# Performance work log

Hardware: AMD Instinct MI355X
Metric: run time of the kernel (lower is better)

Reference implementation:

```python
import jax, jax.numpy as jnp
import numpy as np

N = 50000       # nodes
E = 800000      # edges (avg degree 16)
C_IN = 128
C_HID = 64
C_OUT = 64
NEG_SLOPE = 0.2  # PyG GATConv default


def setup_inputs() -> dict:
    key = jax.random.key(0)
    ks = jax.random.split(key, 20)
    inp = {
        "x": jax.random.normal(ks[0], (N, C_IN), dtype=jnp.float32),
        "edge_index": jax.random.randint(ks[1], (2, E), 0, N, dtype=jnp.int32),
        "batch_size": N,
        "framework": 1,
    }
    dims = [(C_IN, C_HID), (C_HID, C_HID), (C_HID, C_OUT)]
    k = 2
    for i, (cin, cout) in enumerate(dims):
        s = 1.0 / np.sqrt(cin)
        inp[f"W{i}"] = jax.random.normal(ks[k], (cin, cout), jnp.float32) * s; k += 1
        inp[f"a_src{i}"] = jax.random.normal(ks[k], (cout,), jnp.float32) * (1.0 / np.sqrt(cout)); k += 1
        inp[f"a_dst{i}"] = jax.random.normal(ks[k], (cout,), jnp.float32) * (1.0 / np.sqrt(cout)); k += 1
        inp[f"b{i}"] = jnp.zeros((cout,), jnp.float32); k += 1
    return inp


def _gat_conv(h, src, dst, n, W, a_src, a_dst, b):
    # h: [n, cin] -> [n, cout]; single head, PyG GATConv semantics
    hp = h @ W                                   # [n, cout]
    alpha_s = hp @ a_src                         # [n]
    alpha_d = hp @ a_dst                         # [n]
    e = alpha_s[src] + alpha_d[dst]              # [E'] per-edge logits
    e = jnp.where(e > 0, e, NEG_SLOPE * e)       # leaky_relu(0.2)
    # segment softmax over incoming edges of each destination node
    m = jax.ops.segment_max(e, dst, num_segments=n)
    e = jnp.exp(e - m[dst])
    denom = jax.ops.segment_sum(e, dst, num_segments=n)
    a = e / (denom[dst] + 1e-16)                 # [E']
    msg = hp[src] * a[:, None]                   # [E', cout]
    out = jax.ops.segment_sum(msg, dst, num_segments=n)
    return out + b


def reference(x, edge_index, batch_size, framework,
              W0, a_src0, a_dst0, b0,
              W1, a_src1, a_dst1, b1,
              W2, a_src2, a_dst2, b2):
    n = x.shape[0]
    loops = jnp.arange(n, dtype=edge_index.dtype)  # PyG add_self_loops=True
    src = jnp.concatenate([edge_index[0], loops])
    dst = jnp.concatenate([edge_index[1], loops])
    params = [(W0, a_src0, a_dst0, b0), (W1, a_src1, a_dst1, b1), (W2, a_src2, a_dst2, b2)]
    h = x
    for W, a_s, a_d, b in params:
        h = jax.nn.relu(_gat_conv(h, src, dst, n, W, a_s, a_d, b))
    if framework:
        return h
    return h[:batch_size]
```

## Files before the change

### kernel.cpp

```cpp
#include <hip/hip_runtime.h>
#include <hip/hip_fp16.h>
#include <math.h>

#define NEG_SLOPE 0.2f
#define BSHIFT 8
#define BCAP 8192

typedef __attribute__((ext_vector_type(8))) short bf16x8;
typedef __attribute__((ext_vector_type(4))) float f32x4;

__device__ __forceinline__ float leaky(float e) {
    return e > 0.f ? e : NEG_SLOPE * e;
}
__device__ __forceinline__ float to_f(float x) { return x; }
__device__ __forceinline__ float to_f(__half x) { return __half2float(x); }


__global__ __launch_bounds__(256) void partition_kernel(
        const int* __restrict__ src, const int* __restrict__ dst,
        int* __restrict__ bucketLen, int* __restrict__ pairs, int E, int nbk) {
    __shared__ int cnt[256];
    __shared__ int run[256];
    int t = threadIdx.x;
    int chunk = (E + gridDim.x - 1) / gridDim.x;
    int beg = blockIdx.x * chunk;
    int end = min(beg + chunk, E);
    cnt[t] = 0;
    __syncthreads();
    for (int i = beg + t; i < end; i += 256)
        atomicAdd(&cnt[dst[i] >> BSHIFT], 1);
    __syncthreads();
    if (t < nbk) run[t] = t * BCAP + atomicAdd(&bucketLen[t], cnt[t]);
    __syncthreads();
    for (int i = beg + t; i < end; i += 256) {
        int d = dst[i];
        int slot = atomicAdd(&run[d >> BSHIFT], 1);
        if (slot < (d >> BSHIFT) * BCAP + BCAP)
            pairs[slot] = (src[i] << BSHIFT) | (d & 255);
    }
}

__global__ __launch_bounds__(256) void csr_build_kernel(
        const int* __restrict__ bucketLen, const int* __restrict__ pairs,
        int* __restrict__ off, int* __restrict__ degA,
        int* __restrict__ csr_src, int N, int nbk) {
    __shared__ int degl[256];
    __shared__ int s[256];
    __shared__ int cur[256];
    int t = threadIdx.x;
    int b = blockIdx.x;
    int n0 = b << BSHIFT;
    int nodecnt = min(256, N - n0);
    int ebeg = b * BCAP;
    int eend = ebeg + bucketLen[b];

    degl[t] = 0;
    __syncthreads();
    for (int i = ebeg + t; i < eend; i += 256)
        atomicAdd(&degl[pairs[i] & 255], 1);
    __syncthreads();

    int v = degl[t];
    s[t] = v;
    __syncthreads();
    for (int o = 1; o < 256; o <<= 1) {
        int x = (t >= o) ? s[t - o] : 0;
        __syncthreads();
        s[t] += x;
        __syncthreads();
    }
    int excl = s[t] - v;
    if (t < nodecnt) {
        off[n0 + t] = ebeg + excl;
        degA[n0 + t] = v;
    }
    cur[t] = excl;
    __syncthreads();

    for (int i = ebeg + t; i < eend; i += 256) {
        int pk = pairs[i];
        int p = atomicAdd(&cur[pk & 255], 1);
        csr_src[ebeg + p] = pk >> BSHIFT;
    }
}


__device__ __forceinline__ unsigned f2bf_bits(float x) {
    unsigned u = __float_as_uint(x);
    return (u + 0x7fffu + ((u >> 16) & 1u)) >> 16;
}

__global__ __launch_bounds__(256) void pack_w3_kernel(
        const float* __restrict__ W0, const float* __restrict__ W1,
        const float* __restrict__ W2, short* __restrict__ Whi,
        short* __restrict__ Wlo, int* __restrict__ bucketLen) {
    int idx = blockIdx.x * 256 + threadIdx.x;
    if (idx < 256) bucketLen[idx] = 0;
    if (idx >= 16384) return;
    const float* W;
    int base, li;
    if (idx < 8192)       { W = W0; base = 0;     li = idx; }
    else if (idx < 12288) { W = W1; base = 8192;  li = idx - 8192; }
    else                  { W = W2; base = 12288; li = idx - 12288; }
    int k = li >> 6, col = li & 63;
    int c = k >> 5, kin = k & 31;
    int g = col >> 4, nn = col & 15;
    float x = W[li];
    unsigned hb = f2bf_bits(x);
    float hf = __uint_as_float(hb << 16);
    unsigned lb = f2bf_bits(x - hf);
    int o = base + (((c * 4 + g) * 16 + nn) << 5) + kin;
    Whi[o] = (short)hb;
    Wlo[o] = (short)lb;
}


template <int CIN, typename InT>
__global__ __launch_bounds__(256) void gemm_mfma_kernel(
        const InT* __restrict__ h, const short* __restrict__ Whi,
        const short* __restrict__ Wlo,
        const float* __restrict__ a_src, const float* __restrict__ a_dst,
        __half* __restrict__ hp, float* __restrict__ as_, float* __restrict__ ad_,
        int n) {
    constexpr int KC = CIN / 32;
    int t = threadIdx.x, wave = t >> 6, lane = t & 63;
    int quad = lane >> 4, l16 = lane & 15;
    int node0 = blockIdx.x * 64 + wave * 16;

    f32x4 acc[4];
#pragma unroll
    for (int g = 0; g < 4; ++g) acc[g] = (f32x4){0.f, 0.f, 0.f, 0.f};

    int nodeA = node0 + l16;
    bool va = nodeA < n;
    const InT* hrow = h + (size_t)(va ? nodeA : 0) * CIN + quad * 8;

#pragma unroll
    for (int c = 0; c < KC; ++c) {
        bf16x8 bhi[4], blo[4];
#pragma unroll
        for (int g = 0; g < 4; ++g) {
            int o = (((c * 4 + g) * 16 + l16) << 5) + quad * 8;
            bhi[g] = *(const bf16x8*)(Whi + o);
            blo[g] = *(const bf16x8*)(Wlo + o);
        }
        bf16x8 ahi, alo;
#pragma unroll
        for (int j = 0; j < 8; ++j) {
            float x = va ? to_f(hrow[c * 32 + j]) : 0.f;
            unsigned hb = f2bf_bits(x);
            float hf = __uint_as_float(hb << 16);
            unsigned lb = f2bf_bits(x - hf);
            ahi[j] = (short)hb;
            alo[j] = (short)lb;
        }
#pragma unroll
        for (int g = 0; g < 4; ++g) {
            acc[g] = __builtin_amdgcn_mfma_f32_16x16x32_bf16(ahi, bhi[g], acc[g], 0, 0, 0);
            acc[g] = __builtin_amdgcn_mfma_f32_16x16x32_bf16(ahi, blo[g], acc[g], 0, 0, 0);
            acc[g] = __builtin_amdgcn_mfma_f32_16x16x32_bf16(alo, bhi[g], acc[g], 0, 0, 0);
        }
    }

    float as4[4], ad4[4];
#pragma unroll
    for (int g = 0; g < 4; ++g) {
        as4[g] = a_src[g * 16 + l16];
        ad4[g] = a_dst[g * 16 + l16];
    }
#pragma unroll
    for (int r = 0; r < 4; ++r) {
        int node = node0 + quad * 4 + r;
        bool v = node < n;
        float vs = 0.f, vd = 0.f;
#pragma unroll
        for (int g = 0; g < 4; ++g) {
            float val = acc[g][r];
            if (v) hp[(size_t)node * 64 + g * 16 + l16] = __float2half_rn(val);
            vs = fmaf(val, as4[g], vs);
            vd = fmaf(val, ad4[g], vd);
        }
#pragma unroll
        for (int o = 1; o <= 8; o <<= 1) {
            vs += __shfl_xor(vs, o);
            vd += __shfl_xor(vd, o);
        }
        if (v && l16 == 0) {
            as_[node] = vs;
            ad_[node] = vd;
        }
    }
}


__device__ __forceinline__ void h4_to_f(uint2 u, float* f) {
    __half2 a = *(__half2*)&u.x;
    __half2 b = *(__half2*)&u.y;
    float2 f01 = __half22float2(a);
    float2 f23 = __half22float2(b);
    f[0] = f01.x; f[1] = f01.y; f[2] = f23.x; f[3] = f23.y;
}

__device__ __forceinline__ void store_row(float* out, size_t idx, float4 r) {
    ((float4*)out)[idx] = r;
}
__device__ __forceinline__ void store_row(__half* out, size_t idx, float4 r) {
    __half2 a = __floats2half2_rn(r.x, r.y);
    __half2 b = __floats2half2_rn(r.z, r.w);
    uint2 u;
    u.x = *(unsigned*)&a;
    u.y = *(unsigned*)&b;
    ((uint2*)out)[idx] = u;
}
__device__ __forceinline__ void store_el(float* out, size_t idx, float v) { out[idx] = v; }
__device__ __forceinline__ void store_el(__half* out, size_t idx, float v) { out[idx] = __float2half_rn(v); }

template <typename OutT>
__global__ __launch_bounds__(256) void agg_kernel(
        const __half* __restrict__ hp,
        const float* __restrict__ as_, const float* __restrict__ ad_,
        const int* __restrict__ off, const int* __restrict__ degA,
        const int* __restrict__ csr_src,
        const float* __restrict__ bias, OutT* __restrict__ out, int n) {
    __shared__ float pw[4][64];
    __shared__ int ps[4][64];
    int t = threadIdx.x;
    int wave = t >> 6, lane = t & 63;
    int node = blockIdx.x * 4 + wave;
    if (node >= n) return;

    int beg = off[node];
    int deg = degA[node];
    int end = beg + deg;
    float adst = ad_[node];
    float e_self = leaky(as_[node] + adst);

    if (deg <= 64) {
        bool valid = lane < deg;
        int s = valid ? csr_src[beg + lane] : 0;
        float e = valid ? leaky(as_[s] + adst) : -3.4e38f;

        float m = e;
#pragma unroll
        for (int o = 32; o > 0; o >>= 1) m = fmaxf(m, __shfl_xor(m, o));
        m = fmaxf(m, e_self);

        float p = valid ? __expf(e - m) : 0.f;
        float pself = __expf(e_self - m);
        float se = p;
#pragma unroll
        for (int o = 32; o > 0; o >>= 1) se += __shfl_xor(se, o);
        se += pself;
        float inv = 1.0f / (se + 1e-16f);
        p *= inv;

        pw[wave][lane] = p;
        ps[wave][lane] = s;

        int group = lane >> 4, sub = lane & 15;
        const uint2* hp2 = (const uint2*)hp;

        float wself = (group == 0) ? pself * inv : 0.f;
        float hv[4];
        h4_to_f(hp2[(size_t)node * 16 + sub], hv);
        float ax = wself * hv[0], ay = wself * hv[1];
        float az = wself * hv[2], aw = wself * hv[3];

        int j = group;
        float w0 = 0.f, w1 = 0.f;
        uint2 u0 = make_uint2(0u, 0u), u1 = make_uint2(0u, 0u);
        if (j < deg) {
            w0 = pw[wave][j];
            u0 = hp2[(size_t)ps[wave][j] * 16 + sub];
        }
        if (j + 4 < deg) {
            w1 = pw[wave][j + 4];
            u1 = hp2[(size_t)ps[wave][j + 4] * 16 + sub];
        }
        for (; j + 8 < deg; j += 4) {
            float w2 = pw[wave][j + 8];
            uint2 u2 = hp2[(size_t)ps[wave][j + 8] * 16 + sub];
            float f[4];
            h4_to_f(u0, f);
            ax = fmaf(w0, f[0], ax);
            ay = fmaf(w0, f[1], ay);
            az = fmaf(w0, f[2], az);
            aw = fmaf(w0, f[3], aw);
            w0 = w1; u0 = u1;
            w1 = w2; u1 = u2;
        }
        if (j < deg) {
            float f[4];
            h4_to_f(u0, f);
            ax = fmaf(w0, f[0], ax);
            ay = fmaf(w0, f[1], ay);
            az = fmaf(w0, f[2], az);
            aw = fmaf(w0, f[3], aw);
        }
        if (j + 4 < deg) {
            float f[4];
            h4_to_f(u1, f);
            ax = fmaf(w1, f[0], ax);
            ay = fmaf(w1, f[1], ay);
            az = fmaf(w1, f[2], az);
            aw = fmaf(w1, f[3], aw);
        }

#pragma unroll
        for (int o = 16; o <= 32; o <<= 1) {
            ax += __shfl_xor(ax, o);
            ay += __shfl_xor(ay, o);
            az += __shfl_xor(az, o);
            aw += __shfl_xor(aw, o);
        }

        float4 b4 = ((const float4*)bias)[sub];
        float4 r;
        r.x = ax + b4.x; r.x = r.x > 0.f ? r.x : 0.f;
        r.y = ay + b4.y; r.y = r.y > 0.f ? r.y : 0.f;
        r.z = az + b4.z; r.z = r.z > 0.f ? r.z : 0.f;
        r.w = aw + b4.w; r.w = r.w > 0.f ? r.w : 0.f;
        if (group == 0) store_row(out, (size_t)node * 16 + sub, r);
    } else {
        float mymax = e_self;
        for (int i = beg + lane; i < end; i += 64) {
            int s = csr_src[i];
            mymax = fmaxf(mymax, leaky(as_[s] + adst));
        }
#pragma unroll
        for (int o = 32; o > 0; o >>= 1) mymax = fmaxf(mymax, __shfl_xor(mymax, o));
        float m = mymax;

        float se = 0.f;
        for (int i = beg + lane; i < end; i += 64) {
            int s = csr_src[i];
            se += __expf(leaky(as_[s] + adst) - m);
        }
#pragma unroll
        for (int o = 32; o > 0; o >>= 1) se += __shfl_xor(se, o);
        se += __expf(e_self - m);
        float inv = 1.0f / (se + 1e-16f);

        float acc = __expf(e_self - m) * inv * __half2float(hp[(size_t)node * 64 + lane]);
        for (int i = beg; i < end; ++i) {
            int s = csr_src[i];
            float w = __expf(leaky(as_[s] + adst) - m) * inv;
            acc = fmaf(w, __half2float(hp[(size_t)s * 64 + lane]), acc);
        }
        float r = acc + bias[lane];
        store_el(out, (size_t)node * 64 + lane, r > 0.f ? r : 0.f);
    }
}


extern "C" void kernel_launch(void* const* d_in, const int* in_sizes, int n_in,
                              void* d_out, int out_size, void* d_ws, size_t ws_size,
                              hipStream_t stream) {
    const float* x = (const float*)d_in[0];
    const int* edge_index = (const int*)d_in[1];
    const int N = in_sizes[0] / 128;
    const int E = in_sizes[1] / 2;
    const int NBK = (N + 255) >> BSHIFT;

    const float* W[3]    = {(const float*)d_in[4], (const float*)d_in[8],  (const float*)d_in[12]};
    const float* asrc[3] = {(const float*)d_in[5], (const float*)d_in[9],  (const float*)d_in[13]};
    const float* adst[3] = {(const float*)d_in[6], (const float*)d_in[10], (const float*)d_in[14]};
    const float* bias[3] = {(const float*)d_in[7], (const float*)d_in[11], (const float*)d_in[15]};

    char* ws = (char*)d_ws;
    size_t o = 0;
    auto alloc = [&](size_t bytes) {
        char* p = ws + o;
        o += (bytes + 255) & ~(size_t)255;
        return p;
    };
    int* bucketLen    = (int*)alloc(256 * 4);
    int* pairs        = (int*)alloc((size_t)NBK * BCAP * 4);
    int* off          = (int*)alloc((size_t)N * 4);
    int* degA         = (int*)alloc((size_t)N * 4);
    int* csr_src      = (int*)alloc((size_t)NBK * BCAP * 4);
    float* as_        = (float*)alloc((size_t)N * 4);
    float* ad_        = (float*)alloc((size_t)N * 4);
    __half* hpbuf     = (__half*)alloc((size_t)N * 64 * 2);
    __half* actB      = (__half*)alloc((size_t)N * 64 * 2);
    short* Whi        = (short*)alloc(16384 * 2);
    short* Wlo        = (short*)alloc(16384 * 2);

    const int* srcp = edge_index;
    const int* dstp = edge_index + E;

    pack_w3_kernel<<<64, 256, 0, stream>>>(W[0], W[1], W[2], Whi, Wlo, bucketLen);
    partition_kernel<<<256, 256, 0, stream>>>(srcp, dstp, bucketLen, pairs, E, NBK);
    csr_build_kernel<<<NBK, 256, 0, stream>>>(bucketLen, pairs, off, degA, csr_src, N, NBK);

    int gb = (N + 63) / 64;
    int ab = (N + 3) / 4;

    gemm_mfma_kernel<128, float><<<gb, 256, 0, stream>>>(
        x, Whi, Wlo, asrc[0], adst[0], hpbuf, as_, ad_, N);
    agg_kernel<__half><<<ab, 256, 0, stream>>>(
        hpbuf, as_, ad_, off, degA, csr_src, bias[0], actB, N);

    gemm_mfma_kernel<64, __half><<<gb, 256, 0, stream>>>(
        actB, Whi + 8192, Wlo + 8192, asrc[1], adst[1], hpbuf, as_, ad_, N);
    agg_kernel<__half><<<ab, 256, 0, stream>>>(
        hpbuf, as_, ad_, off, degA, csr_src, bias[1], actB, N);

    gemm_mfma_kernel<64, __half><<<gb, 256, 0, stream>>>(
        actB, Whi + 12288, Wlo + 12288, asrc[2], adst[2], hpbuf, as_, ad_, N);
    agg_kernel<float><<<ab, 256, 0, stream>>>(
        hpbuf, as_, ad_, off, degA, csr_src, bias[2], (float*)d_out, N);
}
```

Before: 272.7 us.

## Fuse CSR build with first GEMM, use half-wave per node in aggregation

Merges the CSR build and the first-layer GEMM into one launch, with blocks split by index so the two independent jobs run side by side. The aggregation kernel now gives each node 32 lanes instead of 64, handling 8 nodes per block, and issues four gathers per step for more memory-level parallelism. The high-degree fallback loads half2 pairs, and the partition grid grows from 256 to 1024 blocks. Half-wave nodes use fewer lanes per gather, and nodes with more than 32 in-edges drop to the slower serial path.

```diff
diff --git a/kernel.cpp b/kernel.cpp
--- a/kernel.cpp
+++ b/kernel.cpp
@@ -40,15 +40,14 @@
     }
 }
 
-__global__ __launch_bounds__(256) void csr_build_kernel(
-        const int* __restrict__ bucketLen, const int* __restrict__ pairs,
+__device__ void csr_build_body(
+        int b, const int* __restrict__ bucketLen, const int* __restrict__ pairs,
         int* __restrict__ off, int* __restrict__ degA,
-        int* __restrict__ csr_src, int N, int nbk) {
+        int* __restrict__ csr_src, int N) {
     __shared__ int degl[256];
     __shared__ int s[256];
     __shared__ int cur[256];
     int t = threadIdx.x;
-    int b = blockIdx.x;
     int n0 = b << BSHIFT;
     int nodecnt = min(256, N - n0);
     int ebeg = b * BCAP;
@@ -116,8 +115,8 @@
 
 
 template <int CIN, typename InT>
-__global__ __launch_bounds__(256) void gemm_mfma_kernel(
-        const InT* __restrict__ h, const short* __restrict__ Whi,
+__device__ void gemm_body(
+        int bid, const InT* __restrict__ h, const short* __restrict__ Whi,
         const short* __restrict__ Wlo,
         const float* __restrict__ a_src, const float* __restrict__ a_dst,
         __half* __restrict__ hp, float* __restrict__ as_, float* __restrict__ ad_,
@@ -125,7 +124,7 @@
     constexpr int KC = CIN / 32;
     int t = threadIdx.x, wave = t >> 6, lane = t & 63;
     int quad = lane >> 4, l16 = lane & 15;
-    int node0 = blockIdx.x * 64 + wave * 16;
+    int node0 = bid * 64 + wave * 16;
 
     f32x4 acc[4];
 #pragma unroll
@@ -190,6 +189,31 @@
             ad_[node] = vd;
         }
     }
+}
+
+__global__ __launch_bounds__(256) void csr_gemm0_kernel(
+        const int* __restrict__ bucketLen, const int* __restrict__ pairs,
+        int* __restrict__ off, int* __restrict__ degA, int* __restrict__ csr_src,
+        int N, int nbk,
+        const float* __restrict__ x, const short* __restrict__ Whi,
+        const short* __restrict__ Wlo, const float* __restrict__ a_src,
+        const float* __restrict__ a_dst, __half* __restrict__ hp,
+        float* __restrict__ as_, float* __restrict__ ad_) {
+    if ((int)blockIdx.x < nbk)
+        csr_build_body(blockIdx.x, bucketLen, pairs, off, degA, csr_src, N);
+    else
+        gemm_body<128, float>((int)blockIdx.x - nbk, x, Whi, Wlo, a_src, a_dst,
+                              hp, as_, ad_, N);
+}
+
+template <int CIN, typename InT>
+__global__ __launch_bounds__(256) void gemm_mfma_kernel(
+        const InT* __restrict__ h, const short* __restrict__ Whi,
+        const short* __restrict__ Wlo,
+        const float* __restrict__ a_src, const float* __restrict__ a_dst,
+        __half* __restrict__ hp, float* __restrict__ as_, float* __restrict__ ad_,
+        int n) {
+    gemm_body<CIN, InT>((int)blockIdx.x, h, Whi, Wlo, a_src, a_dst, hp, as_, ad_, n);
 }
 
 
@@ -226,7 +250,8 @@
     __shared__ int ps[4][64];
     int t = threadIdx.x;
     int wave = t >> 6, lane = t & 63;
-    int node = blockIdx.x * 4 + wave;
+    int hf = lane >> 5, l32 = lane & 31;
+    int node = blockIdx.x * 8 + wave * 2 + hf;
     if (node >= n) return;
 
     int beg = off[node];
@@ -235,21 +260,21 @@
     float adst = ad_[node];
     float e_self = leaky(as_[node] + adst);
 
-    if (deg <= 64) {
-        bool valid = lane < deg;
-        int s = valid ? csr_src[beg + lane] : 0;
+    if (deg <= 32) {
+        bool valid = l32 < deg;
+        int s = valid ? csr_src[beg + l32] : 0;
         float e = valid ? leaky(as_[s] + adst) : -3.4e38f;
 
         float m = e;
 #pragma unroll
-        for (int o = 32; o > 0; o >>= 1) m = fmaxf(m, __shfl_xor(m, o));
+        for (int o = 16; o > 0; o >>= 1) m = fmaxf(m, __shfl_xor(m, o));
         m = fmaxf(m, e_self);
 
         float p = valid ? __expf(e - m) : 0.f;
         float pself = __expf(e_self - m);
         float se = p;
 #pragma unroll
-        for (int o = 32; o > 0; o >>= 1) se += __shfl_xor(se, o);
+        for (int o = 16; o > 0; o >>= 1) se += __shfl_xor(se, o);
         se += pself;
         float inv = 1.0f / (se + 1e-16f);
         p *= inv;
@@ -257,7 +282,7 @@
         pw[wave][lane] = p;
         ps[wave][lane] = s;
 
-        int group = lane >> 4, sub = lane & 15;
+        int group = l32 >> 4, sub = l32 & 15;
         const uint2* hp2 = (const uint2*)hp;
 
         float wself = (group == 0) ? pself * inv : 0.f;
@@ -266,53 +291,33 @@
         float ax = wself * hv[0], ay = wself * hv[1];
         float az = wself * hv[2], aw = wself * hv[3];
 
-        int j = group;
-        float w0 = 0.f, w1 = 0.f;
-        uint2 u0 = make_uint2(0u, 0u), u1 = make_uint2(0u, 0u);
-        if (j < deg) {
-            w0 = pw[wave][j];
-            u0 = hp2[(size_t)ps[wave][j] * 16 + sub];
-        }
-        if (j + 4 < deg) {
-            w1 = pw[wave][j + 4];
-            u1 = hp2[(size_t)ps[wave][j + 4] * 16 + sub];
-        }
-        for (; j + 8 < deg; j += 4) {
-            float w2 = pw[wave][j + 8];
-            uint2 u2 = hp2[(size_t)ps[wave][j + 8] * 16 + sub];
-            float f[4];
-            h4_to_f(u0, f);
-            ax = fmaf(w0, f[0], ax);
-            ay = fmaf(w0, f[1], ay);
-            az = fmaf(w0, f[2], az);
-            aw = fmaf(w0, f[3], aw);
-            w0 = w1; u0 = u1;
-            w1 = w2; u1 = u2;
-        }
-        if (j < deg) {
-            float f[4];
-            h4_to_f(u0, f);
-            ax = fmaf(w0, f[0], ax);
-            ay = fmaf(w0, f[1], ay);
-            az = fmaf(w0, f[2], az);
-            aw = fmaf(w0, f[3], aw);
-        }
-        if (j + 4 < deg) {
-            float f[4];
-            h4_to_f(u1, f);
-            ax = fmaf(w1, f[0], ax);
-            ay = fmaf(w1, f[1], ay);
-            az = fmaf(w1, f[2], az);
-            aw = fmaf(w1, f[3], aw);
-        }
-
-#pragma unroll
-        for (int o = 16; o <= 32; o <<= 1) {
-            ax += __shfl_xor(ax, o);
-            ay += __shfl_xor(ay, o);
-            az += __shfl_xor(az, o);
-            aw += __shfl_xor(aw, o);
-        }
+        int base = hf * 32;
+        for (int j = group; j < deg; j += 8) {
+            float w4[4];
+            uint2 u4[4];
+#pragma unroll
+            for (int q = 0; q < 4; ++q) {
+                int jj = j + 2 * q;
+                bool ok = jj < deg;
+                w4[q] = ok ? pw[wave][base + jj] : 0.f;
+                u4[q] = ok ? hp2[(size_t)ps[wave][base + jj] * 16 + sub]
+                           : make_uint2(0u, 0u);
+            }
+#pragma unroll
+            for (int q = 0; q < 4; ++q) {
+                float f[4];
+                h4_to_f(u4[q], f);
+                ax = fmaf(w4[q], f[0], ax);
+                ay = fmaf(w4[q], f[1], ay);
+                az = fmaf(w4[q], f[2], az);
+                aw = fmaf(w4[q], f[3], aw);
+            }
+        }
+
+        ax += __shfl_xor(ax, 16);
+        ay += __shfl_xor(ay, 16);
+        az += __shfl_xor(az, 16);
+        aw += __shfl_xor(aw, 16);
 
         float4 b4 = ((const float4*)bias)[sub];
         float4 r;
@@ -323,32 +328,39 @@
         if (group == 0) store_row(out, (size_t)node * 16 + sub, r);
     } else {
         float mymax = e_self;
-        for (int i = beg + lane; i < end; i += 64) {
+        for (int i = beg + l32; i < end; i += 32) {
             int s = csr_src[i];
             mymax = fmaxf(mymax, leaky(as_[s] + adst));
         }
 #pragma unroll
-        for (int o = 32; o > 0; o >>= 1) mymax = fmaxf(mymax, __shfl_xor(mymax, o));
+        for (int o = 16; o > 0; o >>= 1) mymax = fmaxf(mymax, __shfl_xor(mymax, o));
         float m = mymax;
 
         float se = 0.f;
-        for (int i = beg + lane; i < end; i += 64) {
+        for (int i = beg + l32; i < end; i += 32) {
             int s = csr_src[i];
             se += __expf(leaky(as_[s] + adst) - m);
         }
 #pragma unroll
-        for (int o = 32; o > 0; o >>= 1) se += __shfl_xor(se, o);
+        for (int o = 16; o > 0; o >>= 1) se += __shfl_xor(se, o);
         se += __expf(e_self - m);
         float inv = 1.0f / (se + 1e-16f);
 
-        float acc = __expf(e_self - m) * inv * __half2float(hp[(size_t)node * 64 + lane]);
+        const __half2* hpx = (const __half2*)hp;
+        float2 hs = __half22float2(hpx[(size_t)node * 32 + l32]);
+        float wself = __expf(e_self - m) * inv;
+        float a0 = wself * hs.x, a1 = wself * hs.y;
         for (int i = beg; i < end; ++i) {
             int s = csr_src[i];
             float w = __expf(leaky(as_[s] + adst) - m) * inv;
-            acc = fmaf(w, __half2float(hp[(size_t)s * 64 + lane]), acc);
-        }
-        float r = acc + bias[lane];
-        store_el(out, (size_t)node * 64 + lane, r > 0.f ? r : 0.f);
+            float2 hv = __half22float2(hpx[(size_t)s * 32 + l32]);
+            a0 = fmaf(w, hv.x, a0);
+            a1 = fmaf(w, hv.y, a1);
+        }
+        float r0 = a0 + bias[l32 * 2];
+        float r1 = a1 + bias[l32 * 2 + 1];
+        store_el(out, (size_t)node * 64 + l32 * 2,     r0 > 0.f ? r0 : 0.f);
+        store_el(out, (size_t)node * 64 + l32 * 2 + 1, r1 > 0.f ? r1 : 0.f);
     }
 }
 
@@ -389,15 +401,15 @@
     const int* srcp = edge_index;
     const int* dstp = edge_index + E;
 
+    int gb = (N + 63) / 64;
+    int ab = (N + 7) / 8;
+
     pack_w3_kernel<<<64, 256, 0, stream>>>(W[0], W[1], W[2], Whi, Wlo, bucketLen);
-    partition_kernel<<<256, 256, 0, stream>>>(srcp, dstp, bucketLen, pairs, E, NBK);
-    csr_build_kernel<<<NBK, 256, 0, stream>>>(bucketLen, pairs, off, degA, csr_src, N, NBK);
-
-    int gb = (N + 63) / 64;
-    int ab = (N + 3) / 4;
-
-    gemm_mfma_kernel<128, float><<<gb, 256, 0, stream>>>(
-        x, Whi, Wlo, asrc[0], adst[0], hpbuf, as_, ad_, N);
+    partition_kernel<<<1024, 256, 0, stream>>>(srcp, dstp, bucketLen, pairs, E, NBK);
+
+    csr_gemm0_kernel<<<NBK + gb, 256, 0, stream>>>(
+        bucketLen, pairs, off, degA, csr_src, N, NBK,
+        x, Whi, Wlo, asrc[0], adst[0], hpbuf, as_, ad_);
     agg_kernel<__half><<<ab, 256, 0, stream>>>(
         hpbuf, as_, ad_, off, degA, csr_src, bias[0], actB, N);
 
```

After: 273.0 us. No clear change (+0.1%).
